# Kernel optimization log

Hardware: AMD Instinct MI355X
Metric: run time of the kernel (lower is better)

## Reference

```python
import jax, jax.numpy as jnp
import numpy as np


def setup_inputs() -> dict:
    key = jax.random.key(0)
    ks = jax.random.split(key, 6)
    B, S, D, H, K = 16384, 16, 256, 128, 32
    s1 = 1.0 / np.sqrt(D)
    s2 = 1.0 / np.sqrt(H)
    s3 = 1.0 / np.sqrt(K)
    return {
        "x": jax.random.normal(ks[0], (B, D), jnp.float32),
        "W1": jax.random.normal(ks[1], (S, D, H), jnp.float32) * s1,
        "b1": jnp.zeros((S, H), jnp.float32),
        "W2": jax.random.normal(ks[2], (S, H, D), jnp.float32) * s2,
        "b2": jnp.zeros((S, D), jnp.float32),
        "Wc1": jax.random.normal(ks[3], (S, D, K), jnp.float32) * s1,
        "bc1": jnp.zeros((S, K), jnp.float32),
        "Wc2": jax.random.normal(ks[4], (S, K), jnp.float32) * s3,
        "bc2": jnp.zeros((S,), jnp.float32),
        "lam": jnp.ones((S,), jnp.float32) / S,  # lambda_weights init = 1/n_sources
    }


def reference(x, W1, b1, W2, b2, Wc1, bc1, Wc2, bc2, lam):
    # Batched per-source 2-layer MLP: [B,D] x [S,D,H] -> [B,S,H]
    h = jax.nn.relu(jnp.einsum("bd,sdh->bsh", x, W1) + b1[None])
    outs = jnp.einsum("bsh,shd->bsd", h, W2) + b2[None]            # [B,S,D]
    # Confidence net on each source output
    ch = jax.nn.relu(jnp.einsum("bsd,sdk->bsk", outs, Wc1) + bc1[None])
    conf = jax.nn.sigmoid(jnp.einsum("bsk,sk->bs", ch, Wc2) + bc2[None])  # [B,S]
    # Weighted, normalized combination
    cw = lam[None, :] * conf                                        # [B,S]
    cw = cw / (cw.sum(axis=1, keepdims=True) + 1e-6)
    out = jnp.einsum("bsd,bs->bd", outs, cw)                        # [B,D]
    return out
```

## Files before the change

kernel.cpp:

```cpp
#include <hip/hip_runtime.h>
#include <math.h>

#define S_N 16
#define D_N 256
#define H_N 128
#define K_N 32
#define BT  64

typedef __attribute__((ext_vector_type(8))) short bf16x8;
typedef __attribute__((ext_vector_type(4))) float f32x4;

#define MFMA(a, b, c) __builtin_amdgcn_mfma_f32_16x16x32_bf16(a, b, c, 0, 0, 0)

static __device__ __forceinline__ unsigned short f2bf(float f) {
  union { float f; unsigned u; } v; v.f = f;
  unsigned r = v.u + 0x7FFFu + ((v.u >> 16) & 1u);
  return (unsigned short)(r >> 16);
}

__global__ __launch_bounds__(256)
void lsi_transpose(const float* __restrict__ W1, const float* __restrict__ W2,
                   unsigned short* __restrict__ W1t,
                   unsigned short* __restrict__ W2t)
{
  __shared__ float t[32][33];
  int bid = blockIdx.x;
  const float* src; unsigned short* dst; int R, C, r0, c0;
  if (bid < 512) {
    int s = bid >> 5, tt = bid & 31;
    R = 256; C = 128; r0 = (tt >> 2) * 32; c0 = (tt & 3) * 32;
    src = W1 + (size_t)s * 256 * 128; dst = W1t + (size_t)s * 128 * 256;
  } else {
    int s = (bid - 512) >> 5, tt = (bid - 512) & 31;
    R = 128; C = 256; r0 = (tt >> 3) * 32; c0 = (tt & 7) * 32;
    src = W2 + (size_t)s * 128 * 256; dst = W2t + (size_t)s * 256 * 128;
  }
  int li = threadIdx.x >> 5, lj = threadIdx.x & 31;
  #pragma unroll
  for (int i = 0; i < 4; ++i)
    t[li + i * 8][lj] = src[(size_t)(r0 + li + i * 8) * C + c0 + lj];
  __syncthreads();
  #pragma unroll
  for (int i = 0; i < 4; ++i)
    dst[(size_t)(c0 + li + i * 8) * R + r0 + lj] = f2bf(t[lj][li + i * 8]);
}

__global__ __launch_bounds__(256)
void lsi_wfuse(const float* __restrict__ W2, const float* __restrict__ Wc1,
               const float* __restrict__ b2, const float* __restrict__ bc1,
               unsigned short* __restrict__ Wft, float* __restrict__ bcf)
{
  __shared__ float wc1s[256 * 32];
  const int s = blockIdx.x, t = threadIdx.x;
  const float* Wc1s = Wc1 + (size_t)s * 256 * 32;
  #pragma unroll
  for (int i = 0; i < 8; ++i)
    *(float4*)&wc1s[(t + i * 256) * 4] = *(const float4*)&Wc1s[(t + i * 256) * 4];
  __syncthreads();

  const int hh = t >> 1, kb = (t & 1) * 16;
  const float* w2r = W2 + (size_t)s * 128 * 256 + (size_t)hh * 256;
  float acc[16];
  #pragma unroll
  for (int j = 0; j < 16; ++j) acc[j] = 0.f;
  for (int d0 = 0; d0 < 256; d0 += 4) {
    float4 w4 = *(const float4*)(w2r + d0);
    #pragma unroll
    for (int dd = 0; dd < 4; ++dd) {
      float wv = ((const float*)&w4)[dd];
      #pragma unroll
      for (int j = 0; j < 16; ++j)
        acc[j] += wv * wc1s[(d0 + dd) * 32 + kb + j];
    }
  }
  #pragma unroll
  for (int j = 0; j < 16; ++j)
    Wft[((size_t)s * K_N + kb + j) * H_N + hh] = f2bf(acc[j]);

  if (t < K_N) {
    float a = bc1[s * K_N + t];
    for (int d = 0; d < 256; ++d)
      a += b2[s * D_N + d] * wc1s[d * 32 + t];
    bcf[s * K_N + t] = a;
  }
}

__global__ __launch_bounds__(512, 2)
void lsi_main(const float* __restrict__ x,
              const float* __restrict__ b1,
              const float* __restrict__ b2,
              const float* __restrict__ Wc2,
              const float* __restrict__ bc2,
              const float* __restrict__ lam,
              const unsigned short* __restrict__ W1t,
              const unsigned short* __restrict__ W2t,
              const unsigned short* __restrict__ Wft,
              const float* __restrict__ bcf,
              float* __restrict__ out)
{
  __shared__ unsigned short x_lds[BT * D_N];
  __shared__ unsigned short h_lds[BT * H_N];
  __shared__ float zp_lds[2][BT];
  __shared__ float cw_lds[BT];
  __shared__ float wsum_lds[BT];

  const int tid = threadIdx.x;
  const int w   = tid >> 6;
  const int l   = tid & 63;
  const int rA  = l & 15;
  const int g   = l >> 4;
  const int k8  = g * 8;
  const int b0  = blockIdx.x * BT;
  const int rt3 = w >> 1;
  const int ct3 = w & 1;

  {
    int row = tid >> 3;
    int c0  = (tid & 7) * 32;
    const float* xr = x + (size_t)(b0 + row) * D_N + c0;
    #pragma unroll
    for (int cc = 0; cc < 4; ++cc) {
      float4 f0 = *(const float4*)(xr + cc * 8);
      float4 f1 = *(const float4*)(xr + cc * 8 + 4);
      bf16x8 u;
      u[0] = f2bf(f0.x); u[1] = f2bf(f0.y); u[2] = f2bf(f0.z); u[3] = f2bf(f0.w);
      u[4] = f2bf(f1.x); u[5] = f2bf(f1.y); u[6] = f2bf(f1.z); u[7] = f2bf(f1.w);
      unsigned off = (unsigned)(row * 512 + (c0 + cc * 8) * 2) ^ (unsigned)((row & 7) << 4);
      *(bf16x8*)((char*)x_lds + off) = u;
    }
  }
  if (tid < BT) wsum_lds[tid] = 0.f;

  f32x4 out_acc[2][4];
  f32x4 acc2[2][4];
  #pragma unroll
  for (int a = 0; a < 2; ++a)
    #pragma unroll
    for (int b = 0; b < 4; ++b)
      out_acc[a][b] = (f32x4){0.f, 0.f, 0.f, 0.f};

  __syncthreads();

  for (int s = 0; s < S_N; ++s) {
    f32x4 acc1[4];
    #pragma unroll
    for (int rt = 0; rt < 4; ++rt) acc1[rt] = (f32x4){0.f, 0.f, 0.f, 0.f};
    {
      const unsigned short* B1 = W1t + ((size_t)s * H_N + w * 16 + rA) * D_N + k8;
      #pragma unroll
      for (int ks = 0; ks < 8; ++ks) {
        bf16x8 bfr = *(const bf16x8*)(B1 + ks * 32);
        #pragma unroll
        for (int rt = 0; rt < 4; ++rt) {
          int row = rt * 16 + rA;
          unsigned off = (unsigned)(row * 512 + (ks * 32 + k8) * 2) ^ (unsigned)((row & 7) << 4);
          bf16x8 afr = *(const bf16x8*)((const char*)x_lds + off);
          acc1[rt] = MFMA(afr, bfr, acc1[rt]);
        }
      }
    }
    if (s > 0) {
      #pragma unroll
      for (int rt = 0; rt < 4; ++rt) {
        f32x4 c4 = *(const f32x4*)&cw_lds[rt * 16 + g * 4];
        #pragma unroll
        for (int i = 0; i < 4; ++i) {
          out_acc[0][rt][i] += c4[i] * acc2[0][rt][i];
          out_acc[1][rt][i] += c4[i] * acc2[1][rt][i];
        }
      }
    }
    {
      const float b1v = b1[s * H_N + w * 16 + rA];
      #pragma unroll
      for (int rt = 0; rt < 4; ++rt)
        #pragma unroll
        for (int i = 0; i < 4; ++i) {
          float v = fmaxf(acc1[rt][i] + b1v, 0.f);
          int row = rt * 16 + g * 4 + i;
          unsigned off = (unsigned)(row * 256 + (w * 16 + rA) * 2) ^ (unsigned)((row & 7) << 4);
          *(unsigned short*)((char*)h_lds + off) = f2bf(v);
        }
    }
    __syncthreads();

    {
      f32x4 acc3 = (f32x4){0.f, 0.f, 0.f, 0.f};
      const unsigned short* Bf = Wft + ((size_t)s * K_N + ct3 * 16 + rA) * H_N + k8;
      #pragma unroll
      for (int ks = 0; ks < 4; ++ks) {
        int row = rt3 * 16 + rA;
        unsigned off = (unsigned)(row * 256 + (ks * 32 + k8) * 2) ^ (unsigned)((row & 7) << 4);
        bf16x8 afr = *(const bf16x8*)((const char*)h_lds + off);
        bf16x8 bfr = *(const bf16x8*)(Bf + ks * 32);
        acc3 = MFMA(afr, bfr, acc3);
      }
      const float bcfv = bcf[s * K_N + ct3 * 16 + rA];
      const float wc2v = Wc2[s * K_N + ct3 * 16 + rA];
      float pz[4];
      #pragma unroll
      for (int i = 0; i < 4; ++i)
        pz[i] = fmaxf(acc3[i] + bcfv, 0.f) * wc2v;
      #pragma unroll
      for (int m = 1; m < 16; m <<= 1)
        #pragma unroll
        for (int i = 0; i < 4; ++i)
          pz[i] += __shfl_xor(pz[i], m);
      if (rA == 0) {
        #pragma unroll
        for (int i = 0; i < 4; ++i)
          zp_lds[ct3][rt3 * 16 + g * 4 + i] = pz[i];
      }
    }
    __syncthreads();

    #pragma unroll
    for (int a = 0; a < 2; ++a)
      #pragma unroll
      for (int b = 0; b < 4; ++b)
        acc2[a][b] = (f32x4){0.f, 0.f, 0.f, 0.f};
    {
      const unsigned short* B2 = W2t + ((size_t)s * D_N + w * 32 + rA) * H_N + k8;
      #pragma unroll
      for (int ks = 0; ks < 4; ++ks) {
        bf16x8 afr[4];
        #pragma unroll
        for (int rt = 0; rt < 4; ++rt) {
          int row = rt * 16 + rA;
          unsigned off = (unsigned)(row * 256 + (ks * 32 + k8) * 2) ^ (unsigned)((row & 7) << 4);
          afr[rt] = *(const bf16x8*)((const char*)h_lds + off);
        }
        #pragma unroll
        for (int ct = 0; ct < 2; ++ct) {
          bf16x8 bfr = *(const bf16x8*)(B2 + ct * 16 * H_N + ks * 32);
          #pragma unroll
          for (int rt = 0; rt < 4; ++rt)
            acc2[ct][rt] = MFMA(afr[rt], bfr, acc2[ct][rt]);
        }
      }
    }
    {
      float b2v0 = b2[s * D_N + w * 32 + rA];
      float b2v1 = b2[s * D_N + w * 32 + 16 + rA];
      #pragma unroll
      for (int rt = 0; rt < 4; ++rt)
        #pragma unroll
        for (int i = 0; i < 4; ++i) {
          acc2[0][rt][i] += b2v0;
          acc2[1][rt][i] += b2v1;
        }
    }
    if (tid < BT) {
      float z  = zp_lds[0][tid] + zp_lds[1][tid] + bc2[s];
      float cv = lam[s] / (1.f + __expf(-z));
      cw_lds[tid] = cv;
      wsum_lds[tid] += cv;
    }
    __syncthreads();
  }

  #pragma unroll
  for (int rt = 0; rt < 4; ++rt) {
    f32x4 c4 = *(const f32x4*)&cw_lds[rt * 16 + g * 4];
    #pragma unroll
    for (int i = 0; i < 4; ++i) {
      out_acc[0][rt][i] += c4[i] * acc2[0][rt][i];
      out_acc[1][rt][i] += c4[i] * acc2[1][rt][i];
    }
  }
  #pragma unroll
  for (int rt = 0; rt < 4; ++rt) {
    f32x4 w4 = *(const f32x4*)&wsum_lds[rt * 16 + g * 4];
    #pragma unroll
    for (int i = 0; i < 4; ++i) {
      int row = rt * 16 + g * 4 + i;
      float winv = 1.f / (w4[i] + 1e-6f);
      out[(size_t)(b0 + row) * D_N + w * 32 + rA]      = out_acc[0][rt][i] * winv;
      out[(size_t)(b0 + row) * D_N + w * 32 + 16 + rA] = out_acc[1][rt][i] * winv;
    }
  }
}

extern "C" void kernel_launch(void* const* d_in, const int* in_sizes, int n_in,
                              void* d_out, int out_size, void* d_ws, size_t ws_size,
                              hipStream_t stream) {
  const float* x   = (const float*)d_in[0];
  const float* W1  = (const float*)d_in[1];
  const float* b1  = (const float*)d_in[2];
  const float* W2  = (const float*)d_in[3];
  const float* b2  = (const float*)d_in[4];
  const float* Wc1 = (const float*)d_in[5];
  const float* bc1 = (const float*)d_in[6];
  const float* Wc2 = (const float*)d_in[7];
  const float* bc2 = (const float*)d_in[8];
  const float* lam = (const float*)d_in[9];
  float* out = (float*)d_out;

  unsigned short* W1t = (unsigned short*)d_ws;
  unsigned short* W2t = W1t + (size_t)S_N * H_N * D_N;
  unsigned short* Wft = W2t + (size_t)S_N * D_N * H_N;
  float*          bcf = (float*)(Wft + (size_t)S_N * K_N * H_N);

  hipLaunchKernelGGL(lsi_transpose, dim3(1024), dim3(256), 0, stream,
                     W1, W2, W1t, W2t);
  hipLaunchKernelGGL(lsi_wfuse, dim3(S_N), dim3(256), 0, stream,
                     W2, Wc1, b2, bc1, Wft, bcf);
  hipLaunchKernelGGL(lsi_main, dim3(16384 / BT), dim3(512), 0, stream,
                     x, b1, b2, Wc2, bc2, lam, W1t, W2t, Wft, bcf, out);
}
```

Before: 132.5 us.

## Split sources across two blocks per row tile and merge prep kernels

The main kernel can now split the 16 sources into two halves handled by separate blocks, doubling the grid from 256 to 512 blocks. Each half writes unnormalized partial outputs and weight sums to workspace, and a new combine kernel adds the halves and normalizes. The confidence computation now runs on 4 waves, which compute the sigmoid weights directly and drop one barrier per source. The transpose and weight-fusion prep kernels are merged into one launch, with the fusion spread over more blocks. The split adds a full-size partial output round trip through memory and an extra launch, and takes the split path only if the workspace is large enough.

```diff
diff --git a/kernel.cpp b/kernel.cpp
--- a/kernel.cpp
+++ b/kernel.cpp
@@ -6,6 +6,7 @@
 #define H_N 128
 #define K_N 32
 #define BT  64
+#define B_N 16384
 
 typedef __attribute__((ext_vector_type(8))) short bf16x8;
 typedef __attribute__((ext_vector_type(4))) float f32x4;
@@ -19,73 +20,62 @@
 }
 
 __global__ __launch_bounds__(256)
-void lsi_transpose(const float* __restrict__ W1, const float* __restrict__ W2,
-                   unsigned short* __restrict__ W1t,
-                   unsigned short* __restrict__ W2t)
+void lsi_prep(const float* __restrict__ W1, const float* __restrict__ W2,
+              const float* __restrict__ Wc1, const float* __restrict__ b2,
+              const float* __restrict__ bc1,
+              unsigned short* __restrict__ W1t,
+              unsigned short* __restrict__ W2t,
+              unsigned short* __restrict__ Wft,
+              float* __restrict__ bcf)
 {
-  __shared__ float t[32][33];
-  int bid = blockIdx.x;
-  const float* src; unsigned short* dst; int R, C, r0, c0;
-  if (bid < 512) {
-    int s = bid >> 5, tt = bid & 31;
-    R = 256; C = 128; r0 = (tt >> 2) * 32; c0 = (tt & 3) * 32;
-    src = W1 + (size_t)s * 256 * 128; dst = W1t + (size_t)s * 128 * 256;
-  } else {
-    int s = (bid - 512) >> 5, tt = (bid - 512) & 31;
-    R = 128; C = 256; r0 = (tt >> 3) * 32; c0 = (tt & 7) * 32;
-    src = W2 + (size_t)s * 128 * 256; dst = W2t + (size_t)s * 256 * 128;
-  }
-  int li = threadIdx.x >> 5, lj = threadIdx.x & 31;
-  #pragma unroll
-  for (int i = 0; i < 4; ++i)
-    t[li + i * 8][lj] = src[(size_t)(r0 + li + i * 8) * C + c0 + lj];
-  __syncthreads();
-  #pragma unroll
-  for (int i = 0; i < 4; ++i)
-    dst[(size_t)(c0 + li + i * 8) * R + r0 + lj] = f2bf(t[lj][li + i * 8]);
-}
-
-__global__ __launch_bounds__(256)
-void lsi_wfuse(const float* __restrict__ W2, const float* __restrict__ Wc1,
-               const float* __restrict__ b2, const float* __restrict__ bc1,
-               unsigned short* __restrict__ Wft, float* __restrict__ bcf)
-{
-  __shared__ float wc1s[256 * 32];
-  const int s = blockIdx.x, t = threadIdx.x;
-  const float* Wc1s = Wc1 + (size_t)s * 256 * 32;
-  #pragma unroll
-  for (int i = 0; i < 8; ++i)
-    *(float4*)&wc1s[(t + i * 256) * 4] = *(const float4*)&Wc1s[(t + i * 256) * 4];
-  __syncthreads();
-
-  const int hh = t >> 1, kb = (t & 1) * 16;
-  const float* w2r = W2 + (size_t)s * 128 * 256 + (size_t)hh * 256;
-  float acc[16];
-  #pragma unroll
-  for (int j = 0; j < 16; ++j) acc[j] = 0.f;
-  for (int d0 = 0; d0 < 256; d0 += 4) {
-    float4 w4 = *(const float4*)(w2r + d0);
-    #pragma unroll
-    for (int dd = 0; dd < 4; ++dd) {
-      float wv = ((const float*)&w4)[dd];
-      #pragma unroll
-      for (int j = 0; j < 16; ++j)
-        acc[j] += wv * wc1s[(d0 + dd) * 32 + kb + j];
-    }
-  }
-  #pragma unroll
-  for (int j = 0; j < 16; ++j)
-    Wft[((size_t)s * K_N + kb + j) * H_N + hh] = f2bf(acc[j]);
-
-  if (t < K_N) {
+  const int bid = blockIdx.x;
+  if (bid < 1024) {
+    __shared__ float t[32][33];
+    const float* src; unsigned short* dst; int R, C, r0, c0;
+    if (bid < 512) {
+      int s = bid >> 5, tt = bid & 31;
+      R = 256; C = 128; r0 = (tt >> 2) * 32; c0 = (tt & 3) * 32;
+      src = W1 + (size_t)s * 256 * 128; dst = W1t + (size_t)s * 128 * 256;
+    } else {
+      int s = (bid - 512) >> 5, tt = (bid - 512) & 31;
+      R = 128; C = 256; r0 = (tt >> 3) * 32; c0 = (tt & 7) * 32;
+      src = W2 + (size_t)s * 128 * 256; dst = W2t + (size_t)s * 256 * 128;
+    }
+    int li = threadIdx.x >> 5, lj = threadIdx.x & 31;
+    #pragma unroll
+    for (int i = 0; i < 4; ++i)
+      t[li + i * 8][lj] = src[(size_t)(r0 + li + i * 8) * C + c0 + lj];
+    __syncthreads();
+    #pragma unroll
+    for (int i = 0; i < 4; ++i)
+      dst[(size_t)(c0 + li + i * 8) * R + r0 + lj] = f2bf(t[lj][li + i * 8]);
+    return;
+  }
+  const int q  = bid - 1024;
+  const int s  = q >> 3, hb = q & 7;
+  const int t  = threadIdx.x;
+  const int hh = hb * 16 + (t >> 4);
+  const int kb = (t & 15) * 2;
+  const float* w2r = W2 + ((size_t)s * H_N + hh) * D_N;
+  const float* wc1 = Wc1 + (size_t)s * D_N * K_N;
+  float a0 = 0.f, a1 = 0.f;
+  for (int d = 0; d < D_N; ++d) {
+    float wv = w2r[d];
+    a0 = fmaf(wv, wc1[d * K_N + kb], a0);
+    a1 = fmaf(wv, wc1[d * K_N + kb + 1], a1);
+  }
+  Wft[((size_t)s * K_N + kb) * H_N + hh]     = f2bf(a0);
+  Wft[((size_t)s * K_N + kb + 1) * H_N + hh] = f2bf(a1);
+  if (hb == 0 && t < K_N) {
     float a = bc1[s * K_N + t];
-    for (int d = 0; d < 256; ++d)
-      a += b2[s * D_N + d] * wc1s[d * 32 + t];
+    for (int d = 0; d < D_N; ++d)
+      a = fmaf(b2[s * D_N + d], wc1[d * K_N + t], a);
     bcf[s * K_N + t] = a;
   }
 }
 
-__global__ __launch_bounds__(512, 2)
+template<int SPLIT>
+__global__ __launch_bounds__(512, SPLIT ? 4 : 2)
 void lsi_main(const float* __restrict__ x,
               const float* __restrict__ b1,
               const float* __restrict__ b2,
@@ -96,11 +86,11 @@
               const unsigned short* __restrict__ W2t,
               const unsigned short* __restrict__ Wft,
               const float* __restrict__ bcf,
-              float* __restrict__ out)
+              float* __restrict__ outp,
+              float* __restrict__ pwsum)
 {
   __shared__ unsigned short x_lds[BT * D_N];
   __shared__ unsigned short h_lds[BT * H_N];
-  __shared__ float zp_lds[2][BT];
   __shared__ float cw_lds[BT];
   __shared__ float wsum_lds[BT];
 
@@ -110,9 +100,11 @@
   const int rA  = l & 15;
   const int g   = l >> 4;
   const int k8  = g * 8;
-  const int b0  = blockIdx.x * BT;
-  const int rt3 = w >> 1;
-  const int ct3 = w & 1;
+
+  int rb, half, s0, ns;
+  if (SPLIT) { rb = blockIdx.x & 255; half = blockIdx.x >> 8; s0 = half * 8; ns = 8; }
+  else       { rb = blockIdx.x;       half = 0;               s0 = 0;        ns = 16; }
+  const int b0 = rb * BT;
 
   {
     int row = tid >> 3;
@@ -141,7 +133,9 @@
 
   __syncthreads();
 
-  for (int s = 0; s < S_N; ++s) {
+  for (int si = 0; si < ns; ++si) {
+    const int s = s0 + si;
+
     f32x4 acc1[4];
     #pragma unroll
     for (int rt = 0; rt < 4; ++rt) acc1[rt] = (f32x4){0.f, 0.f, 0.f, 0.f};
@@ -159,7 +153,7 @@
         }
       }
     }
-    if (s > 0) {
+    if (si > 0) {
       #pragma unroll
       for (int rt = 0; rt < 4; ++rt) {
         f32x4 c4 = *(const f32x4*)&cw_lds[rt * 16 + g * 4];
@@ -184,35 +178,41 @@
     }
     __syncthreads();
 
-    {
-      f32x4 acc3 = (f32x4){0.f, 0.f, 0.f, 0.f};
-      const unsigned short* Bf = Wft + ((size_t)s * K_N + ct3 * 16 + rA) * H_N + k8;
+    if (w < 4) {
+      f32x4 acc3[2];
+      acc3[0] = (f32x4){0.f, 0.f, 0.f, 0.f};
+      acc3[1] = (f32x4){0.f, 0.f, 0.f, 0.f};
+      const unsigned short* Bf = Wft + ((size_t)s * K_N + rA) * H_N + k8;
       #pragma unroll
       for (int ks = 0; ks < 4; ++ks) {
-        int row = rt3 * 16 + rA;
+        int row = w * 16 + rA;
         unsigned off = (unsigned)(row * 256 + (ks * 32 + k8) * 2) ^ (unsigned)((row & 7) << 4);
         bf16x8 afr = *(const bf16x8*)((const char*)h_lds + off);
-        bf16x8 bfr = *(const bf16x8*)(Bf + ks * 32);
-        acc3 = MFMA(afr, bfr, acc3);
-      }
-      const float bcfv = bcf[s * K_N + ct3 * 16 + rA];
-      const float wc2v = Wc2[s * K_N + ct3 * 16 + rA];
+        acc3[0] = MFMA(afr, *(const bf16x8*)(Bf + ks * 32), acc3[0]);
+        acc3[1] = MFMA(afr, *(const bf16x8*)(Bf + 16 * H_N + ks * 32), acc3[1]);
+      }
+      const float bcf0 = bcf[s * K_N + rA],      bcf1 = bcf[s * K_N + 16 + rA];
+      const float wc20 = Wc2[s * K_N + rA],      wc21 = Wc2[s * K_N + 16 + rA];
       float pz[4];
       #pragma unroll
       for (int i = 0; i < 4; ++i)
-        pz[i] = fmaxf(acc3[i] + bcfv, 0.f) * wc2v;
+        pz[i] = fmaxf(acc3[0][i] + bcf0, 0.f) * wc20 +
+                fmaxf(acc3[1][i] + bcf1, 0.f) * wc21;
       #pragma unroll
       for (int m = 1; m < 16; m <<= 1)
         #pragma unroll
         for (int i = 0; i < 4; ++i)
           pz[i] += __shfl_xor(pz[i], m);
       if (rA == 0) {
-        #pragma unroll
-        for (int i = 0; i < 4; ++i)
-          zp_lds[ct3][rt3 * 16 + g * 4 + i] = pz[i];
-      }
-    }
-    __syncthreads();
+        const float lam_s = lam[s], bc2_s = bc2[s];
+        #pragma unroll
+        for (int i = 0; i < 4; ++i) {
+          float cv = lam_s / (1.f + __expf(-(pz[i] + bc2_s)));
+          cw_lds[w * 16 + g * 4 + i] = cv;
+          wsum_lds[w * 16 + g * 4 + i] += cv;
+        }
+      }
+    }
 
     #pragma unroll
     for (int a = 0; a < 2; ++a)
@@ -250,12 +250,6 @@
           acc2[1][rt][i] += b2v1;
         }
     }
-    if (tid < BT) {
-      float z  = zp_lds[0][tid] + zp_lds[1][tid] + bc2[s];
-      float cv = lam[s] / (1.f + __expf(-z));
-      cw_lds[tid] = cv;
-      wsum_lds[tid] += cv;
-    }
     __syncthreads();
   }
 
@@ -268,17 +262,46 @@
       out_acc[1][rt][i] += c4[i] * acc2[1][rt][i];
     }
   }
+  if (SPLIT) {
+    float* po = outp + (size_t)half * B_N * D_N;
+    #pragma unroll
+    for (int rt = 0; rt < 4; ++rt)
+      #pragma unroll
+      for (int i = 0; i < 4; ++i) {
+        int row = rt * 16 + g * 4 + i;
+        po[(size_t)(b0 + row) * D_N + w * 32 + rA]      = out_acc[0][rt][i];
+        po[(size_t)(b0 + row) * D_N + w * 32 + 16 + rA] = out_acc[1][rt][i];
+      }
+    if (tid < BT) pwsum[half * B_N + b0 + tid] = wsum_lds[tid];
+  } else {
+    #pragma unroll
+    for (int rt = 0; rt < 4; ++rt) {
+      f32x4 w4 = *(const f32x4*)&wsum_lds[rt * 16 + g * 4];
+      #pragma unroll
+      for (int i = 0; i < 4; ++i) {
+        int row = rt * 16 + g * 4 + i;
+        float winv = 1.f / (w4[i] + 1e-6f);
+        outp[(size_t)(b0 + row) * D_N + w * 32 + rA]      = out_acc[0][rt][i] * winv;
+        outp[(size_t)(b0 + row) * D_N + w * 32 + 16 + rA] = out_acc[1][rt][i] * winv;
+      }
+    }
+  }
+}
+
+__global__ __launch_bounds__(256)
+void lsi_combine(const float* __restrict__ pout, const float* __restrict__ pwsum,
+                 float* __restrict__ out)
+{
+  size_t i4 = ((size_t)blockIdx.x * 256 + threadIdx.x) * 4;
+  int row = (int)(i4 >> 8);
+  f32x4 a = *(const f32x4*)(pout + i4);
+  f32x4 b = *(const f32x4*)(pout + (size_t)B_N * D_N + i4);
+  float ws = pwsum[row] + pwsum[B_N + row];
+  float inv = 1.f / (ws + 1e-6f);
+  f32x4 r;
   #pragma unroll
-  for (int rt = 0; rt < 4; ++rt) {
-    f32x4 w4 = *(const f32x4*)&wsum_lds[rt * 16 + g * 4];
-    #pragma unroll
-    for (int i = 0; i < 4; ++i) {
-      int row = rt * 16 + g * 4 + i;
-      float winv = 1.f / (w4[i] + 1e-6f);
-      out[(size_t)(b0 + row) * D_N + w * 32 + rA]      = out_acc[0][rt][i] * winv;
-      out[(size_t)(b0 + row) * D_N + w * 32 + 16 + rA] = out_acc[1][rt][i] * winv;
-    }
-  }
+  for (int i = 0; i < 4; ++i) r[i] = (a[i] + b[i]) * inv;
+  *(f32x4*)(out + i4) = r;
 }
 
 extern "C" void kernel_launch(void* const* d_in, const int* in_sizes, int n_in,
@@ -299,12 +322,19 @@
   unsigned short* W1t = (unsigned short*)d_ws;
   unsigned short* W2t = W1t + (size_t)S_N * H_N * D_N;
   unsigned short* Wft = W2t + (size_t)S_N * D_N * H_N;
-  float*          bcf = (float*)(Wft + (size_t)S_N * K_N * H_N);
-
-  hipLaunchKernelGGL(lsi_transpose, dim3(1024), dim3(256), 0, stream,
-                     W1, W2, W1t, W2t);
-  hipLaunchKernelGGL(lsi_wfuse, dim3(S_N), dim3(256), 0, stream,
-                     W2, Wc1, b2, bc1, Wft, bcf);
-  hipLaunchKernelGGL(lsi_main, dim3(16384 / BT), dim3(512), 0, stream,
-                     x, b1, b2, Wc2, bc2, lam, W1t, W2t, Wft, bcf, out);
-}
+  float* bcf   = (float*)(Wft + (size_t)S_N * K_N * H_N);
+  float* pwsum = bcf + S_N * K_N;
+  float* pout  = pwsum + 2 * B_N;
+  size_t need = (size_t)((char*)(pout + (size_t)2 * B_N * D_N) - (char*)d_ws);
+
+  lsi_prep<<<dim3(1152), dim3(256), 0, stream>>>(W1, W2, Wc1, b2, bc1,
+                                                 W1t, W2t, Wft, bcf);
+  if (ws_size >= need) {
+    lsi_main<1><<<dim3(512), dim3(512), 0, stream>>>(x, b1, b2, Wc2, bc2, lam,
+                                                     W1t, W2t, Wft, bcf, pout, pwsum);
+    lsi_combine<<<dim3((B_N * D_N) / 1024), dim3(256), 0, stream>>>(pout, pwsum, out);
+  } else {
+    lsi_main<0><<<dim3(256), dim3(512), 0, stream>>>(x, b1, b2, Wc2, bc2, lam,
+                                                     W1t, W2t, Wft, bcf, out, nullptr);
+  }
+}
```

Result: slower. 212.7 us (+60.6%).
